# Kernel tuning notes

Hardware: AMD Instinct MI355X
Metric: run time of the kernel (lower is better)

## Reference

```python
import jax, jax.numpy as jnp
import numpy as np

EPS = 1e-8
K_SLOTS, D_SLOT, D_FEAT, D_HID, D_MLP, N_ITER = 8, 256, 768, 256, 256, 3
SCALE = D_HID ** -0.5


def _ln(x, g, b):
    m = jnp.mean(x, axis=-1, keepdims=True)
    v = jnp.var(x, axis=-1, keepdims=True)
    return (x - m) * jax.lax.rsqrt(v + 1e-5) * g + b


def setup_inputs() -> dict:
    key = jax.random.key(0)
    ks = jax.random.split(key, 16)
    s = lambda k, shape, fan: jax.random.normal(k, shape, jnp.float32) * (fan ** -0.5)
    return {
        "features": jax.random.normal(ks[0], (32, 4096, D_FEAT), jnp.float32),
        "prev_slots": jax.random.normal(ks[1], (32, K_SLOTS, D_SLOT), jnp.float32),
        "g_in": jnp.ones((D_FEAT,), jnp.float32), "b_in": jnp.zeros((D_FEAT,), jnp.float32),
        "g_s": jnp.ones((D_SLOT,), jnp.float32), "b_s": jnp.zeros((D_SLOT,), jnp.float32),
        "g_m": jnp.ones((D_SLOT,), jnp.float32), "b_m": jnp.zeros((D_SLOT,), jnp.float32),
        "Wq": s(ks[2], (D_HID, D_SLOT), D_SLOT),
        "Wk": s(ks[3], (D_HID, D_FEAT), D_FEAT),
        "Wv": s(ks[4], (D_SLOT, D_FEAT), D_FEAT),
        "W_ih": s(ks[5], (3 * D_SLOT, D_SLOT), D_SLOT),
        "W_hh": s(ks[6], (3 * D_SLOT, D_SLOT), D_SLOT),
        "b_ih": jnp.zeros((3 * D_SLOT,), jnp.float32),
        "b_hh": jnp.zeros((3 * D_SLOT,), jnp.float32),
        "W1": s(ks[7], (D_MLP, D_SLOT), D_SLOT), "b1": jnp.zeros((D_MLP,), jnp.float32),
        "W2": s(ks[8], (D_SLOT, D_MLP), D_MLP), "b2": jnp.zeros((D_SLOT,), jnp.float32),
    }


def reference(features, prev_slots, g_in, b_in, g_s, b_s, g_m, b_m,
              Wq, Wk, Wv, W_ih, W_hh, b_ih, b_hh, W1, b1, W2, b2):
    # features: (B, N, D_feat); prev_slots: (B, K, D_slot)
    fn = _ln(features, g_in, b_in)
    k = jnp.einsum('bnf,hf->bnh', fn, Wk)   # (B, N, H)
    v = jnp.einsum('bnf,df->bnd', fn, Wv)   # (B, N, D_slot)

    def attn_of(slots):
        q = jnp.einsum('bkd,hd->bkh', _ln(slots, g_s, b_s), Wq)
        logits = jnp.einsum('bkh,bnh->bkn', q, k) * SCALE
        return jax.nn.softmax(logits, axis=1)  # softmax over slot axis K

    slots = prev_slots
    for _ in range(N_ITER):
        attn = attn_of(slots)
        attn_n = attn / (jnp.sum(attn, axis=-1, keepdims=True) + EPS)
        updates = jnp.einsum('bkn,bnd->bkd', attn_n, v)
        # torch GRUCell (gates ordered r, z, n)
        gi = jnp.einsum('bkd,gd->bkg', updates, W_ih) + b_ih
        gh = jnp.einsum('bkd,gd->bkg', slots, W_hh) + b_hh
        gi_r, gi_z, gi_n = jnp.split(gi, 3, axis=-1)
        gh_r, gh_z, gh_n = jnp.split(gh, 3, axis=-1)
        r = jax.nn.sigmoid(gi_r + gh_r)
        z = jax.nn.sigmoid(gi_z + gh_z)
        n = jnp.tanh(gi_n + r * gh_n)
        h = (1.0 - z) * n + z * slots
        mlp = jnp.einsum('bkm,dm->bkd',
                         jax.nn.relu(jnp.einsum('bkd,md->bkm', _ln(h, g_m, b_m), W1) + b1),
                         W2) + b2
        slots = h + mlp

    attn_final = attn_of(slots)  # (B, K, N)
    # TTT3R confidence-weighted blend with previous slots
    mask = jax.nn.sigmoid(jnp.mean(attn_final, axis=-1))[..., None]  # (B, K, 1)
    slots_out = slots * mask + prev_slots * (1.0 - mask)
    return slots_out, attn_final
```

## Files before the change

kernel.cpp:

```cpp
#include <hip/hip_runtime.h>

typedef unsigned int uint;
typedef unsigned short ushort;
typedef __bf16 bf16x8 __attribute__((ext_vector_type(8)));
typedef float f32x4 __attribute__((ext_vector_type(4)));

#define B_SZ 32
#define N_SEQ 4096
#define ROWS (B_SZ * N_SEQ)
#define LN_EPS 1e-5f
#define EPS_SUM 1e-8f
#define QSCALE 0.0625f

__device__ inline float u2f(uint x){ union{uint u; float f;} c; c.u = x; return c.f; }
__device__ inline ushort f2bf(float f){
  union{float f; uint u;} c; c.f = f; uint u = c.u;
  return (ushort)((u + 0x7fffu + ((u >> 16) & 1u)) >> 16);
}
__device__ inline uint pack2(float a, float b){ return (uint)f2bf(a) | ((uint)f2bf(b) << 16); }
__device__ inline void unpk8(uint4 u, float* o){
  o[0]=u2f(u.x<<16); o[1]=u2f(u.x&0xffff0000u);
  o[2]=u2f(u.y<<16); o[3]=u2f(u.y&0xffff0000u);
  o[4]=u2f(u.z<<16); o[5]=u2f(u.z&0xffff0000u);
  o[6]=u2f(u.w<<16); o[7]=u2f(u.w&0xffff0000u);
}
__device__ inline f32x4 mfma16(bf16x8 a, bf16x8 b, f32x4 c){
  return __builtin_amdgcn_mfma_f32_16x16x32_bf16(a, b, c, 0, 0, 0);
}
typedef const __attribute__((address_space(1))) void ga_void;
typedef __attribute__((address_space(3))) void ls_void;
__device__ inline void gll16(const void* g, void* l){
  __builtin_amdgcn_global_load_lds((ga_void*)g, (ls_void*)l, 16, 0, 0);
}

__global__ __launch_bounds__(256) void prep_kernel(
    const float* Wk, const float* Wv, const float* g_in, const float* b_in,
    const float* W_ih, const float* W_hh, const float* W1, const float* W2, const float* Wq,
    const float* prev_slots,
    ushort* Wg, ushort* Wihb, ushort* Whhb, ushort* W1b, ushort* W2b, ushort* Wqb,
    float* wb, float* wg, float* slots, ushort* qb)
{
  __shared__ float ra[4], rb[4];
  int blk = blockIdx.x, t = threadIdx.x;
  if (blk < 1536){
    int idx = blk*256 + t;
    int o = idx / 768, f = idx - o*768;
    float w = (o < 256) ? Wk[o*768 + f] : Wv[(o-256)*768 + f];
    Wg[idx] = f2bf(w * g_in[f]);
  } else if (blk < 2304){
    int idx = (blk-1536)*256 + t; Wihb[idx] = f2bf(W_ih[idx]);
  } else if (blk < 3072){
    int idx = (blk-2304)*256 + t; Whhb[idx] = f2bf(W_hh[idx]);
  } else if (blk < 3328){
    int idx = (blk-3072)*256 + t; W1b[idx] = f2bf(W1[idx]);
  } else if (blk < 3584){
    int idx = (blk-3328)*256 + t; W2b[idx] = f2bf(W2[idx]);
  } else if (blk < 3840){
    int idx = (blk-3584)*256 + t; Wqb[idx] = f2bf(Wq[idx]);
  } else if (blk < 4352){
    int o = blk - 3840;
    float ab = 0.f, ag = 0.f;
    for (int i = 0; i < 3; ++i){
      int f = t + 256*i;
      float w = (o < 256) ? Wk[o*768 + f] : Wv[(o-256)*768 + f];
      ab += w * b_in[f]; ag += w * g_in[f];
    }
    int lane = t & 63, wv = t >> 6;
    for (int off = 1; off < 64; off <<= 1){ ab += __shfl_xor(ab, off); ag += __shfl_xor(ag, off); }
    if (lane == 0){ ra[wv] = ab; rb[wv] = ag; }
    __syncthreads();
    if (t == 0){ wb[o] = ra[0]+ra[1]+ra[2]+ra[3]; wg[o] = rb[0]+rb[1]+rb[2]+rb[3]; }
  } else if (blk < 4608){
    int idx = (blk-4352)*256 + t; slots[idx] = prev_slots[idx];
  } else {
    int idx = (blk-4608)*256 + t;
    int b = idx >> 11, rem = idx & 2047, rr = rem >> 8, d = rem & 255;
    qb[b*4096 + (8+rr)*256 + d] = 0;
  }
}

__global__ __launch_bounds__(256) void cvt_stats_kernel(
    const float* feat, ushort* featb, float* meanv, float* rstdv)
{
  int t = threadIdx.x, w = t >> 6, lane = t & 63;
  int row = blockIdx.x*4 + w;
  const float4* fp = (const float4*)(feat + (size_t)row * 768);
  uint2* ob = (uint2*)(featb + (size_t)row * 768);
  float s = 0.f, q = 0.f;
  #pragma unroll
  for (int i = 0; i < 3; ++i){
    float4 v = fp[lane + 64*i];
    s += v.x + v.y + v.z + v.w;
    q += v.x*v.x + v.y*v.y + v.z*v.z + v.w*v.w;
    uint2 pk; pk.x = pack2(v.x, v.y); pk.y = pack2(v.z, v.w);
    ob[lane + 64*i] = pk;
  }
  for (int off = 1; off < 64; off <<= 1){ s += __shfl_xor(s, off); q += __shfl_xor(q, off); }
  if (lane == 0){
    float m = s * (1.f/768.f);
    meanv[row] = m;
    rstdv[row] = rsqrtf(q * (1.f/768.f) - m*m + LN_EPS);
  }
}

__global__ __launch_bounds__(256) void kv_gemm(
    const ushort* featb, const ushort* Wg, const float* wb, const float* wg,
    const float* meanv, const float* rstdv, ushort* kv)
{
  int r0 = blockIdx.x * 128, c0 = blockIdx.y * 128;
  int t = threadIdx.x, w = t >> 6, lane = t & 63, m16 = lane & 15, quad = lane >> 4;
  __shared__ __align__(16) ushort As[128*64];
  __shared__ __align__(16) ushort Bs[128*64];
  __shared__ float mr_m[128], mr_r[128], wbl[128], wgl[128];
  if (t < 128){
    mr_m[t] = meanv[r0 + t]; mr_r[t] = rstdv[r0 + t];
    wbl[t] = wb[c0 + t];     wgl[t] = wg[c0 + t];
  }
  int wr = (w >> 1) * 64, wc = (w & 1) * 64;
  int srow = t >> 3, skc = t & 7;

  f32x4 acc[4][4];
  #pragma unroll
  for (int i = 0; i < 4; ++i)
    #pragma unroll
    for (int j = 0; j < 4; ++j) acc[i][j] = (f32x4){0.f,0.f,0.f,0.f};

  for (int k0 = 0; k0 < 768; k0 += 64){
    if (k0) __syncthreads();
    #pragma unroll
    for (int i = 0; i < 4; ++i){
      int row = srow + i*32;
      int kcg = skc ^ (row & 7);
      gll16(featb + (size_t)(r0+row)*768 + k0 + kcg*8, As + (i*256 + w*64)*8);
    }
    #pragma unroll
    for (int i = 0; i < 4; ++i){
      int col = srow + i*32;
      int kcg = skc ^ (col & 7);
      gll16(Wg + (size_t)(c0+col)*768 + k0 + kcg*8, Bs + (i*256 + w*64)*8);
    }
    __syncthreads();
    bf16x8 af[4][2], bfr[4][2];
    #pragma unroll
    for (int i = 0; i < 4; ++i){
      int row = wr + 16*i + m16;
      #pragma unroll
      for (int h = 0; h < 2; ++h){
        int kc = (quad + h*4) ^ (row & 7);
        af[i][h] = __builtin_bit_cast(bf16x8, *(const uint4*)&As[(row*8 + kc)*8]);
      }
    }
    #pragma unroll
    for (int j = 0; j < 4; ++j){
      int col = wc + 16*j + m16;
      #pragma unroll
      for (int h = 0; h < 2; ++h){
        int kc = (quad + h*4) ^ (col & 7);
        bfr[j][h] = __builtin_bit_cast(bf16x8, *(const uint4*)&Bs[(col*8 + kc)*8]);
      }
    }
    #pragma unroll
    for (int j = 0; j < 4; ++j)
      #pragma unroll
      for (int i = 0; i < 4; ++i){
        acc[i][j] = mfma16(af[i][0], bfr[j][0], acc[i][j]);
        acc[i][j] = mfma16(af[i][1], bfr[j][1], acc[i][j]);
      }
  }
  #pragma unroll
  for (int i = 0; i < 4; ++i){
    #pragma unroll
    for (int j = 0; j < 4; ++j){
      int col = wc + 16*j + m16;
      float wgc = wgl[col], wbc = wbl[col];
      f32x4 c = acc[i][j];
      #pragma unroll
      for (int r = 0; r < 4; ++r){
        int row = wr + 16*i + quad*4 + r;
        float val = mr_r[row] * (c[r] - mr_m[row]*wgc) + wbc;
        kv[(size_t)(r0+row)*512 + c0 + col] = f2bf(val);
      }
    }
  }
}

__global__ __launch_bounds__(256) void q_kernel(
    const float* slots, const ushort* Wqb, const float* g_s, const float* b_s, ushort* qb)
{
  int blk = blockIdx.x; int b = blk >> 3, kk = blk & 7;
  int t = threadIdx.x, lane = t & 63, w = t >> 6;
  __shared__ __align__(16) float ln_l[256];
  __shared__ float ra[4], rb[4];
  float x = slots[blk*256 + t];
  float s = x, q = x*x;
  for (int off = 1; off < 64; off <<= 1){ s += __shfl_xor(s, off); q += __shfl_xor(q, off); }
  if (lane == 0){ ra[w] = s; rb[w] = q; }
  __syncthreads();
  float S = ra[0]+ra[1]+ra[2]+ra[3], Q = rb[0]+rb[1]+rb[2]+rb[3];
  float mean = S * (1.f/256.f);
  float rstd = rsqrtf(Q * (1.f/256.f) - mean*mean + LN_EPS);
  ln_l[t] = (x - mean)*rstd*g_s[t] + b_s[t];
  __syncthreads();
  float acc = 0.f;
  const uint4* wq = (const uint4*)(Wqb + (size_t)t*256);
  for (int c = 0; c < 32; ++c){
    float wf[8]; unpk8(wq[c], wf);
    const float* lp = &ln_l[c*8];
    #pragma unroll
    for (int j = 0; j < 8; ++j) acc += wf[j]*lp[j];
  }
  qb[(size_t)(b*16 + kk)*256 + t] = f2bf(acc * QSCALE);
}

__global__ __launch_bounds__(256) void attn_kernel(
    const ushort* kv, const ushort* qb,
    float* upd_part, float* sum_part, float* attn_out, int mode)
{
  int chunk = blockIdx.x, b = blockIdx.y;
  int t = threadIdx.x, w = t >> 6, lane = t & 63, m16 = lane & 15, quad = lane >> 4;
  int n0 = chunk * 256;
  __shared__ __align__(16) float PT[256*9];
  __shared__ float wsum[4][8];
  __shared__ __align__(16) float red[8*2048];

  bf16x8 af[8];
  {
    const uint4* qp = (const uint4*)(qb + ((size_t)(b*16 + m16))*256);
    #pragma unroll
    for (int ks = 0; ks < 8; ++ks) af[ks] = __builtin_bit_cast(bf16x8, qp[ks*4 + quad]);
  }
  const ushort* kvb = kv + ((size_t)(b*4096 + n0))*512;
  f32x4 acc[4];
  #pragma unroll
  for (int nf = 0; nf < 4; ++nf) acc[nf] = (f32x4){0.f,0.f,0.f,0.f};
  #pragma unroll
  for (int ks = 0; ks < 8; ++ks){
    #pragma unroll
    for (int nf = 0; nf < 4; ++nf){
      const uint4* bp = (const uint4*)(kvb + ((size_t)(w*64 + nf*16 + m16))*512);
      bf16x8 bv = __builtin_bit_cast(bf16x8, bp[ks*4 + quad]);
      acc[nf] = mfma16(af[ks], bv, acc[nf]);
    }
  }
  float sacc[4] = {0.f,0.f,0.f,0.f};
  #pragma unroll
  for (int nf = 0; nf < 4; ++nf){
    float l0 = acc[nf][0], l1 = acc[nf][1], l2 = acc[nf][2], l3 = acc[nf][3];
    float mx = fmaxf(fmaxf(l0,l1), fmaxf(l2,l3));
    mx = fmaxf(mx, __shfl_xor(mx, 16));
    float e0 = __expf(l0-mx), e1 = __expf(l1-mx), e2 = __expf(l2-mx), e3 = __expf(l3-mx);
    float s = e0+e1+e2+e3;
    s += __shfl_xor(s, 16);
    float inv = 1.f / s;
    e0 *= inv; e1 *= inv; e2 *= inv; e3 *= inv;
    if (quad < 2){
      sacc[0]+=e0; sacc[1]+=e1; sacc[2]+=e2; sacc[3]+=e3;
      int pos = w*64 + nf*16 + m16;
      if (mode == 0){
        PT[pos*9 + quad*4 + 0] = e0;
        PT[pos*9 + quad*4 + 1] = e1;
        PT[pos*9 + quad*4 + 2] = e2;
        PT[pos*9 + quad*4 + 3] = e3;
      } else {
        int slot = quad*4;
        attn_out[((size_t)(b*8 + slot+0))*4096 + n0 + pos] = e0;
        attn_out[((size_t)(b*8 + slot+1))*4096 + n0 + pos] = e1;
        attn_out[((size_t)(b*8 + slot+2))*4096 + n0 + pos] = e2;
        attn_out[((size_t)(b*8 + slot+3))*4096 + n0 + pos] = e3;
      }
    }
  }
  for (int off = 1; off < 16; off <<= 1){
    sacc[0] += __shfl_xor(sacc[0], off);
    sacc[1] += __shfl_xor(sacc[1], off);
    sacc[2] += __shfl_xor(sacc[2], off);
    sacc[3] += __shfl_xor(sacc[3], off);
  }
  if (m16 == 0 && quad < 2){
    wsum[w][quad*4+0] = sacc[0]; wsum[w][quad*4+1] = sacc[1];
    wsum[w][quad*4+2] = sacc[2]; wsum[w][quad*4+3] = sacc[3];
  }
  __syncthreads();
  if (t < 8){
    float s = wsum[0][t] + wsum[1][t] + wsum[2][t] + wsum[3][t];
    sum_part[(b*16 + chunk)*8 + t] = s;
  }
  if (mode) return;
  int dg = t & 31, pg = t >> 5;
  float ua[8][8];
  #pragma unroll
  for (int k = 0; k < 8; ++k)
    #pragma unroll
    for (int j = 0; j < 8; ++j) ua[k][j] = 0.f;
  const ushort* vb = kv + ((size_t)(b*4096 + n0))*512 + 256;
  for (int i = 0; i < 32; ++i){
    int p = pg*32 + i;
    uint4 vv = *(const uint4*)(vb + (size_t)p*512 + dg*8);
    float vf[8]; unpk8(vv, vf);
    #pragma unroll
    for (int k = 0; k < 8; ++k){
      float a = PT[p*9 + k];
      #pragma unroll
      for (int j = 0; j < 8; ++j) ua[k][j] += a * vf[j];
    }
  }
  #pragma unroll
  for (int k = 0; k < 8; ++k){
    *(float4*)&red[pg*2048 + k*256 + dg*8]     = make_float4(ua[k][0],ua[k][1],ua[k][2],ua[k][3]);
    *(float4*)&red[pg*2048 + k*256 + dg*8 + 4] = make_float4(ua[k][4],ua[k][5],ua[k][6],ua[k][7]);
  }
  __syncthreads();
  #pragma unroll
  for (int j = 0; j < 8; ++j){
    float s = 0.f;
    #pragma unroll
    for (int pgi = 0; pgi < 8; ++pgi) s += red[pgi*2048 + j*256 + t];
    upd_part[((size_t)((b*16 + chunk)*8 + j))*256 + t] = s;
  }
}

__global__ __launch_bounds__(256) void gru_kernel(
    const float* upd_part, const float* sum_part, float* slots,
    const ushort* Wihb, const ushort* Whhb, const ushort* W1b, const ushort* W2b,
    const float* b_ih, const float* b_hh, const float* g_m, const float* b_m,
    const float* b1, const float* b2)
{
  int blk = blockIdx.x; int b = blk >> 3, k = blk & 7;
  int t = threadIdx.x, lane = t & 63, w = t >> 6;
  __shared__ __align__(16) float u_l[256], s_l[256], lnh[256], m1_l[256];
  __shared__ float ra[4], rb[4];
  float stot = EPS_SUM;
  for (int c = 0; c < 16; ++c) stot += sum_part[(b*16 + c)*8 + k];
  float us = 0.f;
  for (int c = 0; c < 16; ++c) us += upd_part[((size_t)((b*16 + c)*8 + k))*256 + t];
  u_l[t] = us / stot;
  s_l[t] = slots[blk*256 + t];
  __syncthreads();
  float gi[3], gh[3];
  for (int gg = 0; gg < 3; ++gg){
    int g = gg*256 + t;
    float ai = b_ih[g], ah = b_hh[g];
    const uint4* wi = (const uint4*)(Wihb + (size_t)g*256);
    const uint4* wh = (const uint4*)(Whhb + (size_t)g*256);
    for (int c = 0; c < 32; ++c){
      float wf[8], hf[8];
      unpk8(wi[c], wf); unpk8(wh[c], hf);
      const float* up = &u_l[c*8];
      const float* sp = &s_l[c*8];
      #pragma unroll
      for (int j = 0; j < 8; ++j){ ai += wf[j]*up[j]; ah += hf[j]*sp[j]; }
    }
    gi[gg] = ai; gh[gg] = ah;
  }
  float r = 1.f/(1.f + __expf(-(gi[0] + gh[0])));
  float z = 1.f/(1.f + __expf(-(gi[1] + gh[1])));
  float n = tanhf(gi[2] + r*gh[2]);
  float h = (1.f - z)*n + z*s_l[t];
  float s = h, q = h*h;
  for (int off = 1; off < 64; off <<= 1){ s += __shfl_xor(s, off); q += __shfl_xor(q, off); }
  if (lane == 0){ ra[w] = s; rb[w] = q; }
  __syncthreads();
  float S = ra[0]+ra[1]+ra[2]+ra[3], Q = rb[0]+rb[1]+rb[2]+rb[3];
  float mean = S * (1.f/256.f);
  float rstd = rsqrtf(Q * (1.f/256.f) - mean*mean + LN_EPS);
  lnh[t] = (h - mean)*rstd*g_m[t] + b_m[t];
  __syncthreads();
  float a1 = b1[t];
  {
    const uint4* w1 = (const uint4*)(W1b + (size_t)t*256);
    for (int c = 0; c < 32; ++c){
      float wf[8]; unpk8(w1[c], wf);
      const float* lp = &lnh[c*8];
      #pragma unroll
      for (int j = 0; j < 8; ++j) a1 += wf[j]*lp[j];
    }
  }
  m1_l[t] = fmaxf(a1, 0.f);
  __syncthreads();
  float a2 = b2[t];
  {
    const uint4* w2 = (const uint4*)(W2b + (size_t)t*256);
    for (int c = 0; c < 32; ++c){
      float wf[8]; unpk8(w2[c], wf);
      const float* mp = &m1_l[c*8];
      #pragma unroll
      for (int j = 0; j < 8; ++j) a2 += wf[j]*mp[j];
    }
  }
  slots[blk*256 + t] = h + a2;
}

__global__ __launch_bounds__(256) void blend_kernel(
    const float* slots, const float* prev, const float* sum_part, float* out)
{
  int blk = blockIdx.x; int b = blk >> 3, k = blk & 7;
  int t = threadIdx.x;
  float s = 0.f;
  for (int c = 0; c < 16; ++c) s += sum_part[(b*16 + c)*8 + k];
  float mean = s * (1.f/4096.f);
  float mask = 1.f/(1.f + __expf(-mean));
  int idx = blk*256 + t;
  out[idx] = slots[idx]*mask + prev[idx]*(1.f - mask);
}

extern "C" void kernel_launch(void* const* d_in, const int* in_sizes, int n_in,
                              void* d_out, int out_size, void* d_ws, size_t ws_size,
                              hipStream_t stream)
{
  (void)in_sizes; (void)n_in; (void)out_size; (void)ws_size;
  const float* feat = (const float*)d_in[0];
  const float* prev = (const float*)d_in[1];
  const float* g_in = (const float*)d_in[2];
  const float* b_in = (const float*)d_in[3];
  const float* g_s  = (const float*)d_in[4];
  const float* b_s  = (const float*)d_in[5];
  const float* g_m  = (const float*)d_in[6];
  const float* b_m  = (const float*)d_in[7];
  const float* Wq   = (const float*)d_in[8];
  const float* Wk   = (const float*)d_in[9];
  const float* Wv   = (const float*)d_in[10];
  const float* W_ih = (const float*)d_in[11];
  const float* W_hh = (const float*)d_in[12];
  const float* b_ih = (const float*)d_in[13];
  const float* b_hh = (const float*)d_in[14];
  const float* W1   = (const float*)d_in[15];
  const float* b1   = (const float*)d_in[16];
  const float* W2   = (const float*)d_in[17];
  const float* b2   = (const float*)d_in[18];
  float* out = (float*)d_out;

  char* ws = (char*)d_ws;
  size_t off = 0;
  auto alloc = [&](size_t bytes)->void*{
    void* p = ws + off;
    off = (off + bytes + 255) & ~(size_t)255;
    return p;
  };
  ushort* kv    = (ushort*)alloc((size_t)ROWS*512*2);
  ushort* featb = (ushort*)alloc((size_t)ROWS*768*2);
  ushort* Wg    = (ushort*)alloc((size_t)512*768*2);
  float*  wbv   = (float*) alloc(512*4);
  float*  wgv   = (float*) alloc(512*4);
  float*  meanv = (float*) alloc((size_t)ROWS*4);
  float*  rstdv = (float*) alloc((size_t)ROWS*4);
  ushort* Wihb  = (ushort*)alloc((size_t)768*256*2);
  ushort* Whhb  = (ushort*)alloc((size_t)768*256*2);
  ushort* W1b   = (ushort*)alloc((size_t)256*256*2);
  ushort* W2b   = (ushort*)alloc((size_t)256*256*2);
  ushort* Wqb   = (ushort*)alloc((size_t)256*256*2);
  float*  slots = (float*) alloc((size_t)65536*4);
  ushort* qb    = (ushort*)alloc((size_t)32*16*256*2);
  float*  updp  = (float*) alloc((size_t)32*16*8*256*4);
  float*  sump  = (float*) alloc((size_t)32*16*8*4);

  prep_kernel<<<4864, 256, 0, stream>>>(Wk, Wv, g_in, b_in, W_ih, W_hh, W1, W2, Wq, prev,
      Wg, Wihb, Whhb, W1b, W2b, Wqb, wbv, wgv, slots, qb);
  cvt_stats_kernel<<<ROWS/4, 256, 0, stream>>>(feat, featb, meanv, rstdv);
  kv_gemm<<<dim3(ROWS/128, 4), 256, 0, stream>>>(featb, Wg, wbv, wgv, meanv, rstdv, kv);

  float* attn_out = out + 65536;
  for (int it = 0; it < 3; ++it){
    q_kernel<<<256, 256, 0, stream>>>(slots, Wqb, g_s, b_s, qb);
    attn_kernel<<<dim3(16, 32), 256, 0, stream>>>(kv, qb, updp, sump, attn_out, 0);
    gru_kernel<<<256, 256, 0, stream>>>(updp, sump, slots, Wihb, Whhb, W1b, W2b,
        b_ih, b_hh, g_m, b_m, b1, b2);
  }
  q_kernel<<<256, 256, 0, stream>>>(slots, Wqb, g_s, b_s, qb);
  attn_kernel<<<dim3(16, 32), 256, 0, stream>>>(kv, qb, updp, sump, attn_out, 1);
  blend_kernel<<<256, 256, 0, stream>>>(slots, prev, sump, out);
}
```

Before: 972.8 us.

## Split K/V into separate buffers with MFMA-fragment-ordered K layout

The kv_gemm epilogue now stages its output tile in shared memory, then writes K in a tile layout pre-permuted to match the MFMA B-fragment order and writes V to its own contiguous 256-wide buffer. The grid is reordered so the four column blocks of one row tile run adjacently, and launch bounds request two blocks per CU. The attention kernel then reads K fragments with fully coalesced 16-byte loads and V with a tighter stride, instead of strided 512-wide row reads. This costs extra shared memory and a barrier in the GEMM epilogue.

```diff
diff --git a/kernel.cpp b/kernel.cpp
--- a/kernel.cpp
+++ b/kernel.cpp
@@ -103,14 +103,16 @@
   }
 }
 
-__global__ __launch_bounds__(256) void kv_gemm(
+__global__ __launch_bounds__(256, 2) void kv_gemm(
     const ushort* featb, const ushort* Wg, const float* wb, const float* wg,
-    const float* meanv, const float* rstdv, ushort* kv)
-{
-  int r0 = blockIdx.x * 128, c0 = blockIdx.y * 128;
+    const float* meanv, const float* rstdv, ushort* kt, ushort* v)
+{
+  int bx = blockIdx.x;
+  int r0 = blockIdx.y * 128, c0 = bx * 128;
   int t = threadIdx.x, w = t >> 6, lane = t & 63, m16 = lane & 15, quad = lane >> 4;
   __shared__ __align__(16) ushort As[128*64];
   __shared__ __align__(16) ushort Bs[128*64];
+  __shared__ __align__(16) ushort Ct[128*136];
   __shared__ float mr_m[128], mr_r[128], wbl[128], wgl[128];
   if (t < 128){
     mr_m[t] = meanv[r0 + t]; mr_r[t] = rstdv[r0 + t];
@@ -178,8 +180,31 @@
       for (int r = 0; r < 4; ++r){
         int row = wr + 16*i + quad*4 + r;
         float val = mr_r[row] * (c[r] - mr_m[row]*wgc) + wbc;
-        kv[(size_t)(r0+row)*512 + c0 + col] = f2bf(val);
+        Ct[row*136 + col] = f2bf(val);
       }
+    }
+  }
+  __syncthreads();
+  if (bx < 2){
+    int ks_off = bx*4;
+    size_t pt0 = (size_t)(r0 >> 4);
+    #pragma unroll
+    for (int ii = 0; ii < 8; ++ii){
+      int flat = t + 256*ii;
+      int perm = flat & 63, ksl = (flat >> 6) & 3, pt = flat >> 8;
+      int row_l = pt*16 + (perm >> 2);
+      int col_l = ksl*32 + (perm & 3)*8;
+      uint4 cv = *(const uint4*)&Ct[row_l*136 + col_l];
+      *(uint4*)(kt + (((pt0 + pt)*8 + (size_t)(ks_off + ksl))*64 + perm)*8) = cv;
+    }
+  } else {
+    int cstrip = (bx - 2) * 128;
+    #pragma unroll
+    for (int ii = 0; ii < 8; ++ii){
+      int flat = t + 256*ii;
+      int row = flat >> 4, c4 = flat & 15;
+      uint4 cv = *(const uint4*)&Ct[row*136 + c4*8];
+      *(uint4*)(v + ((size_t)(r0 + row))*256 + cstrip + c4*8) = cv;
     }
   }
 }
@@ -213,7 +238,7 @@
 }
 
 __global__ __launch_bounds__(256) void attn_kernel(
-    const ushort* kv, const ushort* qb,
+    const ushort* kt, const ushort* v, const ushort* qb,
     float* upd_part, float* sum_part, float* attn_out, int mode)
 {
   int chunk = blockIdx.x, b = blockIdx.y;
@@ -229,7 +254,7 @@
     #pragma unroll
     for (int ks = 0; ks < 8; ++ks) af[ks] = __builtin_bit_cast(bf16x8, qp[ks*4 + quad]);
   }
-  const ushort* kvb = kv + ((size_t)(b*4096 + n0))*512;
+  const uint4* ktb = (const uint4*)kt + ((size_t)(b*256 + (n0 >> 4)))*8*64;
   f32x4 acc[4];
   #pragma unroll
   for (int nf = 0; nf < 4; ++nf) acc[nf] = (f32x4){0.f,0.f,0.f,0.f};
@@ -237,8 +262,7 @@
   for (int ks = 0; ks < 8; ++ks){
     #pragma unroll
     for (int nf = 0; nf < 4; ++nf){
-      const uint4* bp = (const uint4*)(kvb + ((size_t)(w*64 + nf*16 + m16))*512);
-      bf16x8 bv = __builtin_bit_cast(bf16x8, bp[ks*4 + quad]);
+      bf16x8 bv = __builtin_bit_cast(bf16x8, ktb[(((size_t)(w*4 + nf)*8) + ks)*64 + m16*4 + quad]);
       acc[nf] = mfma16(af[ks], bv, acc[nf]);
     }
   }
@@ -292,10 +316,10 @@
   for (int k = 0; k < 8; ++k)
     #pragma unroll
     for (int j = 0; j < 8; ++j) ua[k][j] = 0.f;
-  const ushort* vb = kv + ((size_t)(b*4096 + n0))*512 + 256;
+  const ushort* vb = v + ((size_t)(b*4096 + n0))*256;
   for (int i = 0; i < 32; ++i){
     int p = pg*32 + i;
-    uint4 vv = *(const uint4*)(vb + (size_t)p*512 + dg*8);
+    uint4 vv = *(const uint4*)(vb + (size_t)p*256 + dg*8);
     float vf[8]; unpk8(vv, vf);
     #pragma unroll
     for (int k = 0; k < 8; ++k){
@@ -436,7 +460,8 @@
     off = (off + bytes + 255) & ~(size_t)255;
     return p;
   };
-  ushort* kv    = (ushort*)alloc((size_t)ROWS*512*2);
+  ushort* kt    = (ushort*)alloc((size_t)ROWS*256*2);
+  ushort* vbuf  = (ushort*)alloc((size_t)ROWS*256*2);
   ushort* featb = (ushort*)alloc((size_t)ROWS*768*2);
   ushort* Wg    = (ushort*)alloc((size_t)512*768*2);
   float*  wbv   = (float*) alloc(512*4);
@@ -456,16 +481,16 @@
   prep_kernel<<<4864, 256, 0, stream>>>(Wk, Wv, g_in, b_in, W_ih, W_hh, W1, W2, Wq, prev,
       Wg, Wihb, Whhb, W1b, W2b, Wqb, wbv, wgv, slots, qb);
   cvt_stats_kernel<<<ROWS/4, 256, 0, stream>>>(feat, featb, meanv, rstdv);
-  kv_gemm<<<dim3(ROWS/128, 4), 256, 0, stream>>>(featb, Wg, wbv, wgv, meanv, rstdv, kv);
+  kv_gemm<<<dim3(4, ROWS/128), 256, 0, stream>>>(featb, Wg, wbv, wgv, meanv, rstdv, kt, vbuf);
 
   float* attn_out = out + 65536;
   for (int it = 0; it < 3; ++it){
     q_kernel<<<256, 256, 0, stream>>>(slots, Wqb, g_s, b_s, qb);
-    attn_kernel<<<dim3(16, 32), 256, 0, stream>>>(kv, qb, updp, sump, attn_out, 0);
+    attn_kernel<<<dim3(16, 32), 256, 0, stream>>>(kt, vbuf, qb, updp, sump, attn_out, 0);
     gru_kernel<<<256, 256, 0, stream>>>(updp, sump, slots, Wihb, Whhb, W1b, W2b,
         b_ih, b_hh, g_m, b_m, b1, b2);
   }
   q_kernel<<<256, 256, 0, stream>>>(slots, Wqb, g_s, b_s, qb);
-  attn_kernel<<<dim3(16, 32), 256, 0, stream>>>(kv, qb, updp, sump, attn_out, 1);
+  attn_kernel<<<dim3(16, 32), 256, 0, stream>>>(kt, vbuf, qb, updp, sump, attn_out, 1);
   blend_kernel<<<256, 256, 0, stream>>>(slots, prev, sump, out);
 }
```

New measurement: 980.3 us. No clear change (+0.8%).
